# Performance work log

Measured on AMD Instinct MI355X. Metric: run time of the kernel, lower is better.

## Reference

```python
import jax, jax.numpy as jnp
import numpy as np

EPS = 1e-9
TOP_K = 2
CAPACITY_FACTOR = 4.0
MIN_EXPERT_CAPACITY = 4


def setup_inputs() -> dict:
    key = jax.random.key(0)
    k1, k2 = jax.random.split(key)
    x = jax.random.normal(k1, (4, 32, 512, 24, 24), dtype=jnp.float32)
    w_gating = jax.random.normal(k2, (512, 16), dtype=jnp.float32)
    return {"x": x, "w_gating": w_gating}


def cumsum_exclusive(t, axis):
    # exclusive cumsum along `axis`: cumsum shifted by one (zero first)
    return jnp.cumsum(t, axis=axis) - t


def reference(x, w_gating):
    T, B, D, H, W = x.shape
    N = H * W                       # group_size (tokens per image)
    E = w_gating.shape[1]           # num_gates / experts
    dt = x.dtype

    # pool over timesteps: (T,B,D,H,W) -> (B,N,D)
    x_tok = x.reshape(T, B, D, N).transpose(0, 1, 3, 2)
    x_pooled = x_tok.mean(axis=0)

    raw_gates = jax.nn.softmax(jnp.einsum('bnd,de->bne', x_pooled, w_gating), axis=-1)

    # --- top-k selection loop (importance=None, so no importance masking) ---
    gates_remaining = raw_gates
    masks, gates, indices = [], [], []
    for k in range(TOP_K):
        index_k = jnp.argmax(gates_remaining, axis=-1)                 # (B,N)
        gate_k = jnp.take_along_axis(gates_remaining, index_k[..., None], axis=-1)[..., 0]
        mask_k = jax.nn.one_hot(index_k, E, dtype=dt)                  # (B,N,E)
        masks.append(mask_k)
        gates.append(gate_k)
        indices.append(index_k)
        gates_remaining = gates_remaining * (1.0 - mask_k)

    gate_sum = sum(gates) + EPS
    gates = [g / gate_sum for g in gates]

    # load-balancing loss
    density_1 = masks[0].mean(axis=-2)          # (B,E)
    density_1_proxy = raw_gates.mean(axis=-2)   # (B,E)
    loss = (density_1_proxy * density_1).mean() * float(E ** 2)

    # policy == 'all': masks unchanged

    expert_capacity = min(N, int(N * CAPACITY_FACTOR / E))
    expert_capacity = max(expert_capacity, MIN_EXPERT_CAPACITY)
    cap_f = float(expert_capacity)

    # --- capacity assignment ---
    cumulative_position = jnp.zeros((B, 1, E), dtype=dt)
    positions = [None] * TOP_K
    for k in range(TOP_K):
        position_k = cumsum_exclusive(masks[k], axis=-2) + cumulative_position
        position_k = position_k * masks[k]
        masks[k] = masks[k] * (position_k < cap_f).astype(dt)
        positions[k] = position_k.sum(axis=-1)                          # (B,N)
        gates[k] = gates[k] * masks[k].sum(axis=-1)
        cumulative_position = cumulative_position + masks[k].sum(axis=-2, keepdims=True)

    # --- combine / dispatch tensors (B, N, E, C) ---
    combine_tensor = jnp.zeros((B, N, E, expert_capacity), dtype=dt)
    for k in range(TOP_K):
        mask_k_flat = masks[k].sum(axis=-1)                             # (B,N)
        expert_oh = jax.nn.one_hot(indices[k], E, dtype=dt)             # (B,N,E)
        # out-of-range positions produce all-zero rows, matching safe_one_hot's slice
        pos_oh = jax.nn.one_hot(positions[k].astype(jnp.int32), expert_capacity, dtype=dt)  # (B,N,C)
        combine_tensor = combine_tensor + (
            (gates[k] * mask_k_flat)[..., None, None]
            * expert_oh[..., None]
            * pos_oh[..., None, :]
        )
    dispatch_tensor = (combine_tensor != 0).astype(dt)
    return dispatch_tensor, combine_tensor, loss
```

## Files before the change

kernel.cpp:

```cpp
#include <hip/hip_runtime.h>

#define TT 4
#define BB 32
#define DD 512
#define NN 576
#define EE 16
#define DC 8
#define DCH 64
#define CC 144
#define ROW (EE*CC)
#define SZ 42467328UL

typedef float f4 __attribute__((ext_vector_type(4)));

__global__ __launch_bounds__(576) void k_part(const float* __restrict__ x,
                                              const float* __restrict__ w,
                                              float* __restrict__ part) {
  const int b  = blockIdx.x;
  const int dc = blockIdx.y;
  const int n  = threadIdx.x;
  const int d0 = dc * DCH;

  float acc[EE];
#pragma unroll
  for (int e = 0; e < EE; ++e) acc[e] = 0.f;

  for (int t = 0; t < TT; ++t) {
    const float* xp = x + (((size_t)t * BB + b) * DD + d0) * NN + n;
    for (int dd = 0; dd < DCH; dd += 8) {
      float xv[8];
#pragma unroll
      for (int u = 0; u < 8; ++u) xv[u] = xp[(size_t)(dd + u) * NN];
#pragma unroll
      for (int u = 0; u < 8; ++u) {
        const float* wd = w + (size_t)(d0 + dd + u) * EE;
#pragma unroll
        for (int e = 0; e < EE; ++e) acc[e] = fmaf(xv[u], wd[e], acc[e]);
      }
    }
  }

  float4* dst4 = (float4*)(part + (((size_t)b * NN + n) * DC + dc) * EE);
#pragma unroll
  for (int q = 0; q < 4; ++q)
    dst4[q] = make_float4(acc[4*q], acc[4*q+1], acc[4*q+2], acc[4*q+3]);
}

__global__ __launch_bounds__(576) void k_gate(const float* __restrict__ part,
                                              float4* __restrict__ info,
                                              float* __restrict__ lossp) {
  const int b = blockIdx.x;
  const int n = threadIdx.x;
  const int wave = n >> 6, lane = n & 63;

  __shared__ float sprox[9][EE];
  __shared__ int   swc1[9][EE];
  __shared__ int   swc2[9][EE];
  __shared__ int   woff1[9][EE];
  __shared__ int   woff2[9][EE];
  __shared__ float sproxTot[EE];
  __shared__ int   scnt0[EE];
  __shared__ int   sbase2[EE];

  float l[EE];
#pragma unroll
  for (int e = 0; e < EE; ++e) l[e] = 0.f;
  {
    const float4* p4 = (const float4*)(part + (size_t)(b * NN + n) * (DC * EE));
#pragma unroll
    for (int dc = 0; dc < DC; ++dc) {
#pragma unroll
      for (int q = 0; q < 4; ++q) {
        float4 v = p4[dc * 4 + q];
        l[4*q+0] += v.x; l[4*q+1] += v.y; l[4*q+2] += v.z; l[4*q+3] += v.w;
      }
    }
#pragma unroll
    for (int e = 0; e < EE; ++e) l[e] *= 0.25f;
  }

  float m = l[0];
#pragma unroll
  for (int e = 1; e < EE; ++e) m = fmaxf(m, l[e]);
  float raw[EE]; float s = 0.f;
#pragma unroll
  for (int e = 0; e < EE; ++e) { raw[e] = expf(l[e] - m); s += raw[e]; }
  float inv = 1.f / s;
#pragma unroll
  for (int e = 0; e < EE; ++e) raw[e] *= inv;

  int e1 = 0; float g1 = raw[0];
#pragma unroll
  for (int e = 1; e < EE; ++e) if (raw[e] > g1) { g1 = raw[e]; e1 = e; }
  int e2 = (e1 == 0) ? 1 : 0; float g2 = raw[e2];
#pragma unroll
  for (int e = 0; e < EE; ++e) if (e != e1 && raw[e] > g2) { g2 = raw[e]; e2 = e; }
  const float denom = g1 + g2 + 1e-9f;
  const float w0 = g1 / denom, w1 = g2 / denom;

  const unsigned long long ltm = (1ull << lane) - 1ull;
  int pre1 = 0, pre2 = 0;
#pragma unroll
  for (int e = 0; e < EE; ++e) {
    unsigned long long m1 = __ballot(e1 == e);
    unsigned long long m2 = __ballot(e2 == e);
    if (lane == 0) { swc1[wave][e] = __popcll(m1); swc2[wave][e] = __popcll(m2); }
    if (e == e1) pre1 = __popcll(m1 & ltm);
    if (e == e2) pre2 = __popcll(m2 & ltm);
  }

#pragma unroll
  for (int e = 0; e < EE; ++e) {
    float v = raw[e];
#pragma unroll
    for (int off = 32; off; off >>= 1) v += __shfl_xor(v, off);
    if (lane == 0) sprox[wave][e] = v;
  }
  __syncthreads();

  if (n < EE) {
    int r1 = 0, r2 = 0; float pv = 0.f;
#pragma unroll
    for (int wv = 0; wv < 9; ++wv) {
      woff1[wv][n] = r1; r1 += swc1[wv][n];
      woff2[wv][n] = r2; r2 += swc2[wv][n];
      pv += sprox[wv][n];
    }
    scnt0[n]    = r1;
    sbase2[n]   = r1 < CC ? r1 : CC;
    sproxTot[n] = pv;
  }
  __syncthreads();

  if (n == 0) {
    float S = 0.f;
    for (int e = 0; e < EE; ++e) S += sproxTot[e] * (float)scnt0[e];
    lossp[b] = S / ((float)NN * (float)NN);
  }

  const int p0 = woff1[wave][e1] + pre1;
  const int p1 = sbase2[e2] + woff2[wave][e2] + pre2;

  const int  pos0 = (p0 < CC) ? (e1 * CC + p0) : -1;
  const int  pos1 = (p1 < CC) ? (e2 * CC + p1) : -1;
  const float w0k = (p0 < CC) ? w0 : 0.f;
  const float w1k = (p1 < CC) ? w1 : 0.f;

  float4 o;
  o.x = __int_as_float(pos0);
  o.y = w0k;
  o.z = __int_as_float(pos1);
  o.w = w1k;
  info[b * NN + n] = o;
}

__global__ __launch_bounds__(576) void k_write(const float4* __restrict__ info,
                                               const float* __restrict__ lossp,
                                               float* __restrict__ out) {
  const int blk  = blockIdx.x;
  const int tid  = threadIdx.x;
  const int tok0 = blk * 8;

  if (blk == 0 && tid == 0) {
    float sv = 0.f;
    for (int b = 0; b < BB; ++b) sv += lossp[b];
    out[2 * SZ] = 0.5f * sv;
  }

  __shared__ float4 sinfo[8];
  if (tid < 8) sinfo[tid] = info[tok0 + tid];
  __syncthreads();

  const int f0 = tid * 4;

#pragma unroll
  for (int it = 0; it < 8; ++it) {
    const float4 inf = sinfo[it];
    const int pos0 = __float_as_int(inf.x);
    const int pos1 = __float_as_int(inf.z);
    f4* disp = (f4*)(out + (size_t)(tok0 + it) * ROW);
    f4 dv = { (f0+0 == pos0 || f0+0 == pos1) ? 1.f : 0.f,
              (f0+1 == pos0 || f0+1 == pos1) ? 1.f : 0.f,
              (f0+2 == pos0 || f0+2 == pos1) ? 1.f : 0.f,
              (f0+3 == pos0 || f0+3 == pos1) ? 1.f : 0.f };
    disp[tid] = dv;
  }

#pragma unroll
  for (int it = 0; it < 8; ++it) {
    const float4 inf = sinfo[it];
    const int   pos0 = __float_as_int(inf.x);
    const float w0   = inf.y;
    const int   pos1 = __float_as_int(inf.z);
    const float w1   = inf.w;
    f4* comb = (f4*)(out + SZ + (size_t)(tok0 + it) * ROW);
    f4 cv = { (f0+0 == pos0) ? w0 : ((f0+0 == pos1) ? w1 : 0.f),
              (f0+1 == pos0) ? w0 : ((f0+1 == pos1) ? w1 : 0.f),
              (f0+2 == pos0) ? w0 : ((f0+2 == pos1) ? w1 : 0.f),
              (f0+3 == pos0) ? w0 : ((f0+3 == pos1) ? w1 : 0.f) };
    comb[tid] = cv;
  }
}

extern "C" void kernel_launch(void* const* d_in, const int* in_sizes, int n_in,
                              void* d_out, int out_size, void* d_ws, size_t ws_size,
                              hipStream_t stream) {
  const float* x = (const float*)d_in[0];
  const float* w = (const float*)d_in[1];
  float* out = (float*)d_out;

  float*  part  = (float*)d_ws;
  float4* info  = (float4*)((char*)d_ws + 9437184);
  float*  lossp = (float*)((char*)d_ws + 9437184 + 294912);

  hipLaunchKernelGGL(k_part,  dim3(BB, DC), dim3(576), 0, stream, x, w, part);
  hipLaunchKernelGGL(k_gate,  dim3(BB),     dim3(576), 0, stream, part, info, lossp);
  hipLaunchKernelGGL(k_write, dim3(BB*NN/8), dim3(576), 0, stream, info, lossp, out);
}
```

Before: 124.7 us.

## Restructure gating projection with vector loads, LDS weights, and nontemporal output stores

The partial-logit kernel now has each thread load float4 chunks of four tokens, sum the four timesteps first, and multiply by gating weights staged in LDS. Four thread groups split the D chunk and reduce their results through shared memory. Separately, the large dispatch/combine writes now use nontemporal stores to avoid polluting caches. The cost is more LDS usage and a reduction step, and only 144 threads write the final partials.

```diff
diff --git a/kernel.cpp b/kernel.cpp
--- a/kernel.cpp
+++ b/kernel.cpp
@@ -16,34 +16,78 @@
 __global__ __launch_bounds__(576) void k_part(const float* __restrict__ x,
                                               const float* __restrict__ w,
                                               float* __restrict__ part) {
-  const int b  = blockIdx.x;
-  const int dc = blockIdx.y;
-  const int n  = threadIdx.x;
-  const int d0 = dc * DCH;
-
-  float acc[EE];
-#pragma unroll
-  for (int e = 0; e < EE; ++e) acc[e] = 0.f;
-
-  for (int t = 0; t < TT; ++t) {
-    const float* xp = x + (((size_t)t * BB + b) * DD + d0) * NN + n;
-    for (int dd = 0; dd < DCH; dd += 8) {
-      float xv[8];
-#pragma unroll
-      for (int u = 0; u < 8; ++u) xv[u] = xp[(size_t)(dd + u) * NN];
-#pragma unroll
-      for (int u = 0; u < 8; ++u) {
-        const float* wd = w + (size_t)(d0 + dd + u) * EE;
-#pragma unroll
-        for (int e = 0; e < EE; ++e) acc[e] = fmaf(xv[u], wd[e], acc[e]);
-      }
-    }
-  }
-
-  float4* dst4 = (float4*)(part + (((size_t)b * NN + n) * DC + dc) * EE);
-#pragma unroll
-  for (int q = 0; q < 4; ++q)
-    dst4[q] = make_float4(acc[4*q], acc[4*q+1], acc[4*q+2], acc[4*q+3]);
+  const int b   = blockIdx.x;
+  const int dc  = blockIdx.y;
+  const int tid = threadIdx.x;
+  const int q   = tid % 144;
+  const int g   = tid / 144;
+  const int d0  = dc * DCH;
+
+  __shared__ f4 wlds[DCH][4];
+  __shared__ f4 redu[3][4][4][144];
+
+  {
+    const f4* wsrc = (const f4*)(w + (size_t)d0 * EE);
+    for (int i = tid; i < DCH * 4; i += 576)
+      ((f4*)wlds)[i] = wsrc[i];
+  }
+  __syncthreads();
+
+  const f4* xq = (const f4*)(x + ((size_t)b * DD + d0) * NN);
+  const size_t TS4 = (size_t)BB * DD * NN / 4;
+
+  f4 acc[4][4];
+#pragma unroll
+  for (int j = 0; j < 4; ++j)
+#pragma unroll
+    for (int r = 0; r < 4; ++r) acc[j][r] = (f4)0.f;
+
+#pragma unroll 2
+  for (int k = 0; k < 16; ++k) {
+    const int dlt = g + 4 * k;
+    const size_t off = (size_t)dlt * 144 + q;
+    const f4 a0 = xq[off];
+    const f4 a1 = xq[off + TS4];
+    const f4 a2 = xq[off + 2 * TS4];
+    const f4 a3 = xq[off + 3 * TS4];
+    const f4 xs = (a0 + a1) + (a2 + a3);
+    const f4 wq0 = wlds[dlt][0];
+    const f4 wq1 = wlds[dlt][1];
+    const f4 wq2 = wlds[dlt][2];
+    const f4 wq3 = wlds[dlt][3];
+#pragma unroll
+    for (int j = 0; j < 4; ++j) {
+      const f4 xsj = xs[j];
+      acc[j][0] += wq0 * xsj;
+      acc[j][1] += wq1 * xsj;
+      acc[j][2] += wq2 * xsj;
+      acc[j][3] += wq3 * xsj;
+    }
+  }
+
+  if (g > 0) {
+#pragma unroll
+    for (int j = 0; j < 4; ++j)
+#pragma unroll
+      for (int r = 0; r < 4; ++r)
+        redu[g - 1][j][r][q] = acc[j][r];
+  }
+  __syncthreads();
+  if (g == 0) {
+#pragma unroll
+    for (int gg = 0; gg < 3; ++gg)
+#pragma unroll
+      for (int j = 0; j < 4; ++j)
+#pragma unroll
+        for (int r = 0; r < 4; ++r)
+          acc[j][r] += redu[gg][j][r][q];
+#pragma unroll
+    for (int j = 0; j < 4; ++j) {
+      f4* dst4 = (f4*)(part + (((size_t)b * NN + 4 * q + j) * DC + dc) * EE);
+#pragma unroll
+      for (int r = 0; r < 4; ++r) dst4[r] = acc[j][r];
+    }
+  }
 }
 
 __global__ __launch_bounds__(576) void k_gate(const float* __restrict__ part,
@@ -183,7 +227,7 @@
               (f0+1 == pos0 || f0+1 == pos1) ? 1.f : 0.f,
               (f0+2 == pos0 || f0+2 == pos1) ? 1.f : 0.f,
               (f0+3 == pos0 || f0+3 == pos1) ? 1.f : 0.f };
-    disp[tid] = dv;
+    __builtin_nontemporal_store(dv, &disp[tid]);
   }
 
 #pragma unroll
@@ -198,7 +242,7 @@
               (f0+1 == pos0) ? w0 : ((f0+1 == pos1) ? w1 : 0.f),
               (f0+2 == pos0) ? w0 : ((f0+2 == pos1) ? w1 : 0.f),
               (f0+3 == pos0) ? w0 : ((f0+3 == pos1) ? w1 : 0.f) };
-    comb[tid] = cv;
+    __builtin_nontemporal_store(cv, &comb[tid]);
   }
 }
 
```

Measured after the change: 112.2 us. -10.0%, faster.
